# Performance work log

Measured on AMD Instinct MI355X. Metric: run time of the kernel, lower is better.

## Reference

```python
import jax, jax.numpy as jnp
import numpy as np
import math

Z, N = 4, 128
EMB, L0, MLPH, GEO = 16, 32, 64, 64
NB, NH = 32, 128
C = MLPH + GEO
BETA, MAXR = 5.0, 10.0
Y0 = 0.5 / math.sqrt(math.pi)  # spherical harmonic l=0


def setup_inputs() -> dict:
    key = jax.random.key(0)
    ks = jax.random.split(key, 24)
    g = lambda i, s: jax.random.normal(ks[i], s, jnp.float32)
    inp = {}
    inp['features'] = jax.random.randint(ks[0], (Z, N, 1), 0, 6)
    inp['geometry'] = g(1, (Z, N, 3))
    inp['mask'] = jnp.ones((Z, N), jnp.float32)
    emb = g(2, (6, EMB))
    inp['emb'] = emb.at[5].set(0.0)  # padding_idx=5
    # radial MLP weights per conv layer (basis->h->h->mul_out*mul_in)
    inp['r0w0'] = g(3, (NB, NH)); inp['r0w1'] = g(4, (NH, NH)); inp['r0w2'] = g(5, (NH, L0 * EMB))
    inp['r1w0'] = g(6, (NB, NH)); inp['r1w1'] = g(7, (NH, NH)); inp['r1w2'] = g(8, (NH, L0 * L0))
    inp['r2w0'] = g(9, (NB, NH)); inp['r2w1'] = g(10, (NH, NH)); inp['r2w2'] = g(11, (NH, MLPH * L0))
    # ResnetPointnet (3 -> GEO per atom, two residual FC blocks)
    inp['pn_w0'] = g(12, (3, GEO)) * 0.3; inp['pn_b0'] = jnp.zeros((GEO,), jnp.float32)
    inp['pn_w1a'] = g(13, (GEO, GEO)) * 0.1; inp['pn_b1a'] = jnp.zeros((GEO,), jnp.float32)
    inp['pn_w1b'] = g(14, (GEO, GEO)) * 0.1; inp['pn_b1b'] = jnp.zeros((GEO,), jnp.float32)
    inp['pn_w2a'] = g(15, (GEO, GEO)) * 0.1; inp['pn_b2a'] = jnp.zeros((GEO,), jnp.float32)
    inp['pn_w2b'] = g(16, (GEO, GEO)) * 0.1; inp['pn_b2b'] = jnp.zeros((GEO,), jnp.float32)
    # output MLP + per-atom BatchNorm1d(natoms) params
    inp['e1_w'] = g(17, (C, C)) * 0.05; inp['e1_b'] = jnp.zeros((C,), jnp.float32)
    inp['bn1_g'] = jnp.ones((N,), jnp.float32); inp['bn1_b'] = jnp.zeros((N,), jnp.float32)
    inp['e2_w'] = g(18, (C, 2 * C)) * 0.05; inp['e2_b'] = jnp.zeros((2 * C,), jnp.float32)
    inp['bn2_g'] = jnp.ones((N,), jnp.float32); inp['bn2_b'] = jnp.zeros((N,), jnp.float32)
    return inp


def _sp(x):
    return jax.nn.softplus(BETA * x) / BETA


def _ssp(x):
    return _sp(x) - math.log(2.0) / BETA


def _leaky(x):
    return jnp.where(x > 0, x, 0.2 * x)


def _radial(radii, w0, w1, w2):
    # CosineBasisModel: smooth cosine^2 bumps then small MLP (e3nn-style /sqrt(fan_in))
    centers = jnp.linspace(0.0, MAXR, NB)
    step = centers[1] - centers[0]
    x = (radii[..., None] - centers) / step
    basis = jnp.where(jnp.abs(x) < 1.0, jnp.cos(0.5 * jnp.pi * x) ** 2, 0.0)  # [z,a,b,NB]
    h = _ssp(basis @ w0 / math.sqrt(NB))
    h = _ssp(h @ w1 / math.sqrt(NH))
    return h @ w2 / math.sqrt(NH)  # [z,a,b,dout*din]


def _bn(x, gamma, beta):
    # torch BatchNorm1d(natoms) on [Z, natoms, C]: normalize over (Z, C) per atom slot
    mu = jnp.mean(x, axis=(0, 2), keepdims=True)
    var = jnp.var(x, axis=(0, 2), keepdims=True)
    xn = (x - mu) * jax.lax.rsqrt(var + 1e-5)
    return xn * gamma[None, :, None] + beta[None, :, None]


def reference(features, geometry, mask, emb,
              r0w0, r0w1, r0w2, r1w0, r1w1, r1w2, r2w0, r2w1, r2w2,
              pn_w0, pn_b0, pn_w1a, pn_b1a, pn_w1b, pn_b1b,
              pn_w2a, pn_b2a, pn_w2b, pn_b2b,
              e1_w, e1_b, bn1_g, bn1_b, e2_w, e2_b, bn2_g, bn2_b):
    # constants(): pairwise geometry, detached in the original
    diff = jax.lax.stop_gradient(geometry[:, None, :, :] - geometry[:, :, None, :])  # [z,a,b,3]
    radii = jnp.linalg.norm(diff, axis=-1)  # [z,a,b]

    # ResnetPointnet: per-atom geometric features
    net = geometry @ pn_w0 + pn_b0
    for (wa, ba, wb, bb) in ((pn_w1a, pn_b1a, pn_w1b, pn_b1b), (pn_w2a, pn_b2a, pn_w2b, pn_b2b)):
        dx = jax.nn.relu(net) @ wa + ba
        dx = jax.nn.relu(dx) @ wb + bb
        net = net + dx
    geo_pn = net * mask[..., None]  # [z,n,GEO]

    # embedding
    f = emb[features[..., 0]]  # [z,n,EMB]

    # equivariant kernel-conv layers; all reps are l=0 so Y = Y0 constant
    dims = ((EMB, L0, r0w0, r0w1, r0w2), (L0, L0, r1w0, r1w1, r1w2), (L0, MLPH, r2w0, r2w1, r2w2))
    for (din, dout, w0, w1, w2) in dims:
        f = f / math.sqrt(N)
        K = _radial(radii, w0, w1, w2).reshape(Z, N, N, dout, din)
        f = jnp.einsum('zabij,zbj,zb->zai', K, f, mask) * Y0
        f = _sp(f)               # GatedBlock with all-scalar Rs -> scalar act only
        f = f * mask[..., None]

    feat = jnp.concatenate([f, geo_pn], axis=2)  # [z,n,C]
    x = _leaky(_bn(feat @ e1_w + e1_b, bn1_g, bn1_b))
    x = _leaky(_bn(x @ e2_w + e2_b, bn2_g, bn2_b))
    out = jnp.sum(x * mask[..., None], axis=1)  # Aggregate(axis=1, sum)
    return out  # [Z, 2*C]
```

## Files before the change

### kernel.cpp

```cpp
#include <hip/hip_runtime.h>
#include <math.h>

#define Zc   4
#define Nc   128
#define EMBc 16
#define L0c  32
#define MLPHc 64
#define GEOc 64
#define NBc  32
#define NHc  128
#define Cc   128
#define SLc  64

typedef float  f32x4  __attribute__((ext_vector_type(4)));
typedef short  bf16x8 __attribute__((ext_vector_type(8)));

union FragU {
    bf16x8 v;
    unsigned short u[8];
    uint2 q2[2];
};

__device__ __forceinline__ float sp5(float x){
    float y = 5.0f * x;
    float t = fabsf(y);
    return (fmaxf(y, 0.0f) + log1pf(__expf(-t))) * 0.2f;
}
__device__ __forceinline__ float ssp5f(float x){
    float y = 5.0f * x;
    float e = __expf(-fabsf(y));
    return (fmaxf(y, 0.0f) + __logf(1.0f + e)) * 0.2f - 0.13862943611198906f;
}

__device__ __forceinline__ unsigned short f2bf(float f){
    unsigned int u = __float_as_uint(f);
    unsigned int r = (u + 0x7FFFu + ((u >> 16) & 1u)) >> 16;
    return (unsigned short)r;
}

__device__ __forceinline__ int kmap(int l, int e){
    return 4*((l >> 4) & 3) + (e & 3) + 16*(e >> 2);
}

__global__ __launch_bounds__(256) void k_packw(
    const float* __restrict__ w00, const float* __restrict__ w10,
    const float* __restrict__ w01, const float* __restrict__ w11,
    const float* __restrict__ w02, const float* __restrict__ w12,
    unsigned short* __restrict__ packs)
{
    int layer = blockIdx.y;
    const float* w0s = (layer == 0) ? w00 : (layer == 1) ? w01 : w02;
    const float* w1s = (layer == 0) ? w10 : (layer == 1) ? w11 : w12;
    unsigned short* p0 = packs + layer*4096;
    unsigned short* p1 = packs + 12288 + layer*16384;
    int idx = blockIdx.x*256 + threadIdx.x;
    if (idx < 4096){
        int t8 = idx >> 9, l = (idx >> 3) & 63, e = idx & 7;
        int k = kmap(l, e);
        int n = (t8 << 4) + (l & 15);
        p0[idx] = f2bf(w0s[k*NHc + n] * 0.17677669529663687f);
    } else {
        int j = idx - 4096;
        int fid = j >> 9, l = (j >> 3) & 63, e = j & 7;
        int kk = fid >> 3, t8 = fid & 7;
        int k = 32*kk + kmap(l, e);
        int n = 16*t8 + (l & 15);
        p1[j] = f2bf(w1s[k*NHc + n] * 0.08838834764831845f);
    }
}

__global__ __launch_bounds__(64) void k_pointnet(
    const float* __restrict__ geom, const float* __restrict__ mask,
    const float* __restrict__ pw0, const float* __restrict__ pb0,
    const float* __restrict__ w1a, const float* __restrict__ b1a,
    const float* __restrict__ w1b, const float* __restrict__ b1b,
    const float* __restrict__ w2a, const float* __restrict__ b2a,
    const float* __restrict__ w2b, const float* __restrict__ b2b,
    const int*   __restrict__ features, const float* __restrict__ emb,
    float* __restrict__ geo_pn, float* __restrict__ f0)
{
    int zn = blockIdx.x;
    int c  = threadIdx.x;
    __shared__ float cur[GEOc];
    __shared__ float tmp[GEOc];
    float gx = geom[zn*3+0], gy = geom[zn*3+1], gz = geom[zn*3+2];
    float v = fmaf(gx, pw0[0*GEOc+c], fmaf(gy, pw0[1*GEOc+c], fmaf(gz, pw0[2*GEOc+c], pb0[c])));
    const float* WA[2] = {w1a, w2a}; const float* BA[2] = {b1a, b2a};
    const float* WB[2] = {w1b, w2b}; const float* BB[2] = {b1b, b2b};
    #pragma unroll
    for (int blk = 0; blk < 2; blk++){
        cur[c] = v;
        __syncthreads();
        float s = BA[blk][c];
        for (int k = 0; k < GEOc; k++) s = fmaf(fmaxf(cur[k], 0.0f), WA[blk][k*GEOc+c], s);
        tmp[c] = s;
        __syncthreads();
        float s2 = BB[blk][c];
        for (int k = 0; k < GEOc; k++) s2 = fmaf(fmaxf(tmp[k], 0.0f), WB[blk][k*GEOc+c], s2);
        v = v + s2;
        __syncthreads();
    }
    geo_pn[zn*GEOc + c] = v * mask[zn];
    if (c < EMBc){
        int fi = features[zn];
        f0[zn*EMBc + c] = emb[fi*EMBc + c];
    }
}

template<int DIN, int DOUT>
__global__ __launch_bounds__(256) void k_gmat(
    const float* __restrict__ f, const float* __restrict__ mask,
    const float* __restrict__ w2, unsigned short* __restrict__ gt)
{
    __shared__ float fsh[8][DIN];
    int t   = threadIdx.x;
    int zb0 = blockIdx.x * 8;
    if (t < 8*DIN){
        int r = t / DIN, j = t % DIN;
        int zb = zb0 + r;
        fsh[r][j] = f[zb*DIN + j] * mask[zb] * 0.0022038655607334227f;
    }
    __syncthreads();
    int mi = blockIdx.y * 256 + t;
    int m_ = mi & (NHc-1);
    int i_ = mi >> 7;
    const float* wrow = w2 + (size_t)(m_*DOUT + i_) * DIN;
    float s[8];
    #pragma unroll
    for (int r = 0; r < 8; r++) s[r] = 0.0f;
    #pragma unroll
    for (int j4 = 0; j4 < DIN/4; j4++){
        float4 w = *reinterpret_cast<const float4*>(&wrow[j4*4]);
        #pragma unroll
        for (int q = 0; q < 4; q++){
            float wv = reinterpret_cast<const float*>(&w)[q];
            int j = j4*4 + q;
            #pragma unroll
            for (int r = 0; r < 8; r++)
                s[r] = fmaf(fsh[r][j], wv, s[r]);
        }
    }
    int z = zb0 >> 7;
    #pragma unroll
    for (int r = 0; r < 8; r++){
        int b = (zb0 + r) & (Nc-1);
        gt[((size_t)z*DOUT + i_)*(Nc*NHc) + b*NHc + m_] = f2bf(s[r]);
    }
}

template<int DIN, int DOUT>
__global__ __launch_bounds__(256) void k_egmat(
    const float* __restrict__ part, const float* __restrict__ mask,
    const float* __restrict__ w2, unsigned short* __restrict__ gt)
{
    __shared__ float fsh[8][DIN];
    int t   = threadIdx.x;
    int zb0 = blockIdx.x * 8;
    for (int idx = t; idx < 8*DIN; idx += 256){
        int r = idx / DIN, j = idx % DIN;
        int zb = zb0 + r;
        float s = 0.0f;
        #pragma unroll
        for (int sl = 0; sl < SLc; sl++)
            s += part[(size_t)sl*(Zc*Nc*DIN) + zb*DIN + j];
        float m = mask[zb];
        fsh[r][j] = sp5(s) * m * m * 0.0022038655607334227f;
    }
    __syncthreads();
    int mi = blockIdx.y * 256 + t;
    int m_ = mi & (NHc-1);
    int i_ = mi >> 7;
    const float* wrow = w2 + (size_t)(m_*DOUT + i_) * DIN;
    float s[8];
    #pragma unroll
    for (int r = 0; r < 8; r++) s[r] = 0.0f;
    #pragma unroll
    for (int j4 = 0; j4 < DIN/4; j4++){
        float4 w = *reinterpret_cast<const float4*>(&wrow[j4*4]);
        #pragma unroll
        for (int q = 0; q < 4; q++){
            float wv = reinterpret_cast<const float*>(&w)[q];
            int j = j4*4 + q;
            #pragma unroll
            for (int r = 0; r < 8; r++)
                s[r] = fmaf(fsh[r][j], wv, s[r]);
        }
    }
    int z = zb0 >> 7;
    #pragma unroll
    for (int r = 0; r < 8; r++){
        int b = (zb0 + r) & (Nc-1);
        gt[((size_t)z*DOUT + i_)*(Nc*NHc) + b*NHc + m_] = f2bf(s[r]);
    }
}

__global__ __launch_bounds__(256) void k_pairmlp(
    const float* __restrict__ geom,
    const unsigned short* __restrict__ packs,
    unsigned short* __restrict__ h2all)
{
    __shared__ unsigned short h1s[64*128];
    char* lb = (char*)h1s;
    int layer = blockIdx.y;
    const unsigned short* wp0 = packs + layer*4096;
    const unsigned short* wp1 = packs + 12288 + layer*16384;
    unsigned short* h2 = h2all + (size_t)layer * (Zc*Nc*Nc*NHc);

    int t   = threadIdx.x;
    int w   = t >> 6;
    int l   = t & 63;
    int g16 = l >> 4;
    int c   = l & 15;
    int p0  = blockIdx.x * 64;
    int z   = p0 >> 14;
    int a   = (p0 >> 7) & 127;
    int b0  = p0 & 127;

    int bp = b0 + 16*w + c;
    float ax = geom[(z*Nc + a)*3 + 0];
    float ay = geom[(z*Nc + a)*3 + 1];
    float az = geom[(z*Nc + a)*3 + 2];
    float dx = geom[(z*Nc + bp)*3 + 0] - ax;
    float dy = geom[(z*Nc + bp)*3 + 1] - ay;
    float dz = geom[(z*Nc + bp)*3 + 2] - az;
    float rm = sqrtf(dx*dx + dy*dy + dz*dz);

    FragU af;
    #pragma unroll
    for (int e = 0; e < 8; e++){
        int k = kmap(l, e);
        float x = rm*3.1f - (float)k;
        float v = 0.0f;
        if (fabsf(x) < 1.0f){ float cc = __cosf(1.57079632679f*x); v = cc*cc; }
        af.u[e] = f2bf(v);
    }

    f32x4 acc[8];
    #pragma unroll
    for (int t8 = 0; t8 < 8; t8++) acc[t8] = (f32x4){0.f,0.f,0.f,0.f};
    #pragma unroll
    for (int t8 = 0; t8 < 8; t8++){
        bf16x8 bf = *reinterpret_cast<const bf16x8*>(wp0 + ((t8*64 + l) << 3));
        acc[t8] = __builtin_amdgcn_mfma_f32_16x16x32_bf16(af.v, bf, acc[t8], 0, 0, 0);
    }
    #pragma unroll
    for (int t8 = 0; t8 < 8; t8++){
        #pragma unroll
        for (int rg = 0; rg < 4; rg++){
            int m = 16*w + 4*g16 + rg;
            int n = 16*t8 + c;
            int off = ((m << 8) + (n << 1)) ^ ((m & 7) << 4);
            *(unsigned short*)(lb + off) = f2bf(ssp5f(acc[t8][rg]));
        }
    }
    __syncthreads();

    f32x4 acc2[8];
    #pragma unroll
    for (int t8 = 0; t8 < 8; t8++) acc2[t8] = (f32x4){0.f,0.f,0.f,0.f};
    int mrow = 16*w + c;
    int sw   = (mrow & 7) << 4;
    #pragma unroll
    for (int kk = 0; kk < 4; kk++){
        int ob = (mrow << 8) + (kk << 6) + (g16 << 3);
        FragU a2;
        a2.q2[0] = *(const uint2*)(lb + (ob ^ sw));
        a2.q2[1] = *(const uint2*)(lb + ((ob + 32) ^ sw));
        #pragma unroll
        for (int t8 = 0; t8 < 8; t8++){
            bf16x8 bf = *reinterpret_cast<const bf16x8*>(wp1 + (((kk*8 + t8)*64 + l) << 3));
            acc2[t8] = __builtin_amdgcn_mfma_f32_16x16x32_bf16(a2.v, bf, acc2[t8], 0, 0, 0);
        }
    }
    size_t rowbase = ((size_t)((z*Nc + a)*Nc + b0)) * NHc;
    #pragma unroll
    for (int t8 = 0; t8 < 8; t8++){
        #pragma unroll
        for (int rg = 0; rg < 4; rg++){
            int m = 16*w + 4*g16 + rg;
            h2[rowbase + (size_t)m*NHc + 16*t8 + c] = f2bf(ssp5f(acc2[t8][rg]));
        }
    }
}

template<int DOUT>
__global__ __launch_bounds__(256) void k_gemm3m(
    const unsigned short* __restrict__ h2, const unsigned short* __restrict__ gt,
    float* __restrict__ partial)
{
    __shared__ unsigned short Ash[64*256];
    __shared__ unsigned short Bsh[DOUT*256];
    int t = threadIdx.x;
    int w = t >> 6, l = t & 63;
    int g16 = l >> 4, c16 = l & 15;
    int s  = blockIdx.x;
    int at = blockIdx.y;
    int z  = blockIdx.z;
    int a0 = at*64;
    int k0 = s*256;

    {
        const unsigned short* src = h2 + ((size_t)(z*Nc + a0))*(Nc*NHc) + k0;
        #pragma unroll
        for (int it = 0; it < 8; it++){
            int idx = it*256 + t;
            int r = idx >> 5, c8 = idx & 31;
            uint4 v = *reinterpret_cast<const uint4*>(src + (size_t)r*(Nc*NHc) + c8*8);
            int byte = (r*512 + c8*16) ^ ((r & 7) << 4);
            *reinterpret_cast<uint4*>((char*)Ash + byte) = v;
        }
    }
    {
        const unsigned short* src = gt + ((size_t)z*DOUT)*(Nc*NHc) + k0;
        #pragma unroll
        for (int it = 0; it < DOUT/8; it++){
            int idx = it*256 + t;
            int r = idx >> 5, c8 = idx & 31;
            uint4 v = *reinterpret_cast<const uint4*>(src + (size_t)r*(Nc*NHc) + c8*8);
            int byte = (r*512 + c8*16) ^ ((r & 7) << 4);
            *reinterpret_cast<uint4*>((char*)Bsh + byte) = v;
        }
    }
    __syncthreads();

    constexpr int NT = DOUT/16;
    f32x4 acc[NT];
    #pragma unroll
    for (int nt = 0; nt < NT; nt++) acc[nt] = (f32x4){0.f,0.f,0.f,0.f};
    char* Ab = (char*)Ash; char* Bb = (char*)Bsh;
    int ar  = 16*w + c16;
    int asw = (ar & 7) << 4;
    #pragma unroll
    for (int ks = 0; ks < 8; ks++){
        FragU afr;
        int abyte = ar*512 + ks*64 + g16*8;
        afr.q2[0] = *(const uint2*)(Ab + (abyte ^ asw));
        afr.q2[1] = *(const uint2*)(Ab + ((abyte + 32) ^ asw));
        #pragma unroll
        for (int nt = 0; nt < NT; nt++){
            int br  = nt*16 + c16;
            int bsw = (br & 7) << 4;
            int bbyte = br*512 + ks*64 + g16*8;
            FragU bfr;
            bfr.q2[0] = *(const uint2*)(Bb + (bbyte ^ bsw));
            bfr.q2[1] = *(const uint2*)(Bb + ((bbyte + 32) ^ bsw));
            acc[nt] = __builtin_amdgcn_mfma_f32_16x16x32_bf16(afr.v, bfr.v, acc[nt], 0, 0, 0);
        }
    }
    #pragma unroll
    for (int nt = 0; nt < NT; nt++){
        #pragma unroll
        for (int rg = 0; rg < 4; rg++){
            int a = a0 + 16*w + 4*g16 + rg;
            int i = nt*16 + c16;
            partial[(((size_t)s*Zc + z)*Nc + a)*DOUT + i] = acc[nt][rg];
        }
    }
}

__global__ __launch_bounds__(128) void k_x1f(
    const float* __restrict__ part, const float* __restrict__ mask,
    const float* __restrict__ geo_pn,
    const float* __restrict__ w, const float* __restrict__ b,
    float* __restrict__ x1)
{
    int zn = blockIdx.x;
    int c  = threadIdx.x;
    __shared__ float feat[Cc];
    float fv;
    if (c < MLPHc){
        float s = 0.0f;
        #pragma unroll
        for (int sl = 0; sl < SLc; sl++)
            s += part[(size_t)sl*(Zc*Nc*MLPHc) + zn*MLPHc + c];
        fv = sp5(s) * mask[zn];
    } else {
        fv = geo_pn[zn*GEOc + (c - MLPHc)];
    }
    feat[c] = fv;
    __syncthreads();
    float s = b[c];
    for (int k = 0; k < Cc; k++) s = fmaf(feat[k], w[k*Cc + c], s);
    x1[zn*Cc + c] = s;
}

__global__ __launch_bounds__(256) void k_bnx2(
    const float* __restrict__ x1, const float* __restrict__ g1,
    const float* __restrict__ b1, const float* __restrict__ e2w,
    const float* __restrict__ e2b, float* __restrict__ x2)
{
    int n = blockIdx.x;
    int t = threadIdx.x;
    __shared__ float xsh[Zc][Cc];
    __shared__ float ssum[4], ssq[4];
    float sum = 0.0f, sq = 0.0f;
    for (int idx = t; idx < Zc*Cc; idx += 256){
        int z = idx >> 7, c = idx & 127;
        float v = x1[((size_t)z*Nc + n)*Cc + c];
        xsh[z][c] = v;
        sum += v; sq += v*v;
    }
    #pragma unroll
    for (int off = 32; off > 0; off >>= 1){
        sum += __shfl_down(sum, off);
        sq  += __shfl_down(sq,  off);
    }
    if ((t & 63) == 0){ ssum[t >> 6] = sum; ssq[t >> 6] = sq; }
    __syncthreads();
    float tot  = ssum[0] + ssum[1] + ssum[2] + ssum[3];
    float totq = ssq[0]  + ssq[1]  + ssq[2]  + ssq[3];
    const float inv = 1.0f / (float)(Zc*Cc);
    float mu   = tot * inv;
    float var  = totq * inv - mu*mu;
    float rstd = rsqrtf(var + 1e-5f);
    float ga = g1[n], be = b1[n];
    for (int idx = t; idx < Zc*Cc; idx += 256){
        int z = idx >> 7, c = idx & 127;
        float v = (xsh[z][c] - mu) * rstd * ga + be;
        xsh[z][c] = v > 0.0f ? v : 0.2f*v;
    }
    __syncthreads();
    #pragma unroll
    for (int z = 0; z < Zc; z++){
        float s = e2b[t];
        for (int k = 0; k < Cc; k++) s = fmaf(xsh[z][k], e2w[k*2*Cc + t], s);
        x2[((size_t)z*Nc + n)*2*Cc + t] = s;
    }
}

template<int CC>
__global__ __launch_bounds__(256) void k_bn(
    float* __restrict__ x, const float* __restrict__ gamma,
    const float* __restrict__ beta)
{
    int n = blockIdx.x;
    int t = threadIdx.x;
    __shared__ float ssum[4], ssq[4];
    float sum = 0.0f, sq = 0.0f;
    for (int idx = t; idx < Zc*CC; idx += 256){
        int z = idx / CC, c = idx % CC;
        float v = x[((size_t)z*Nc + n)*CC + c];
        sum += v; sq += v*v;
    }
    #pragma unroll
    for (int off = 32; off > 0; off >>= 1){
        sum += __shfl_down(sum, off);
        sq  += __shfl_down(sq,  off);
    }
    if ((t & 63) == 0){ ssum[t >> 6] = sum; ssq[t >> 6] = sq; }
    __syncthreads();
    float tot  = ssum[0] + ssum[1] + ssum[2] + ssum[3];
    float totq = ssq[0]  + ssq[1]  + ssq[2]  + ssq[3];
    const float inv = 1.0f / (float)(Zc*CC);
    float mu   = tot * inv;
    float var  = totq * inv - mu*mu;
    float rstd = rsqrtf(var + 1e-5f);
    float ga = gamma[n], be = beta[n];
    for (int idx = t; idx < Zc*CC; idx += 256){
        int z = idx / CC, c = idx % CC;
        size_t o = ((size_t)z*Nc + n)*CC + c;
        float v = (x[o] - mu) * rstd * ga + be;
        x[o] = v > 0.0f ? v : 0.2f*v;
    }
}

__global__ __launch_bounds__(256) void k_out(
    const float* __restrict__ x2n, const float* __restrict__ mask,
    float* __restrict__ out)
{
    int z = blockIdx.x;
    int c = threadIdx.x;
    float s = 0.0f;
    for (int n = 0; n < Nc; n++)
        s += x2n[((size_t)z*Nc + n)*2*Cc + c] * mask[z*Nc + n];
    out[z*2*Cc + c] = s;
}

extern "C" void kernel_launch(void* const* d_in, const int* in_sizes, int n_in,
                              void* d_out, int out_size, void* d_ws, size_t ws_size,
                              hipStream_t stream)
{
    const int*   features = (const int*)  d_in[0];
    const float* geom     = (const float*)d_in[1];
    const float* mask     = (const float*)d_in[2];
    const float* emb      = (const float*)d_in[3];
    const float* rw[3][3] = {
        {(const float*)d_in[4],  (const float*)d_in[5],  (const float*)d_in[6]},
        {(const float*)d_in[7],  (const float*)d_in[8],  (const float*)d_in[9]},
        {(const float*)d_in[10], (const float*)d_in[11], (const float*)d_in[12]}};
    const float* pw0 = (const float*)d_in[13]; const float* pb0 = (const float*)d_in[14];
    const float* w1a = (const float*)d_in[15]; const float* b1a = (const float*)d_in[16];
    const float* w1b = (const float*)d_in[17]; const float* b1b = (const float*)d_in[18];
    const float* w2a = (const float*)d_in[19]; const float* b2a = (const float*)d_in[20];
    const float* w2b = (const float*)d_in[21]; const float* b2b = (const float*)d_in[22];
    const float* e1w = (const float*)d_in[23]; const float* e1b = (const float*)d_in[24];
    const float* bn1g= (const float*)d_in[25]; const float* bn1b= (const float*)d_in[26];
    const float* e2w = (const float*)d_in[27]; const float* e2b = (const float*)d_in[28];
    const float* bn2g= (const float*)d_in[29]; const float* bn2b= (const float*)d_in[30];

    float* ws = (float*)d_ws;
    unsigned short* h2buf = (unsigned short*)ws;
    unsigned short* gt    = (unsigned short*)(ws + 12582912);
    float* part   = ws + 12582912 + 2097152;
    float* f0     = part + 2097152;
    float* geo_pn = f0 + 8192;
    float* x1     = geo_pn + 32768;
    float* x2     = x1 + 65536;
    unsigned short* packs = (unsigned short*)(x2 + 131072);
    (void)ws_size; (void)in_sizes; (void)n_in; (void)out_size;

    const size_t H2L = (size_t)Zc*Nc*Nc*NHc;

    k_packw<<<dim3(80, 3), 256, 0, stream>>>(rw[0][0], rw[0][1], rw[1][0], rw[1][1],
                                             rw[2][0], rw[2][1], packs);
    k_pointnet<<<Zc*Nc, 64, 0, stream>>>(geom, mask, pw0, pb0, w1a, b1a, w1b, b1b,
                                         w2a, b2a, w2b, b2b, features, emb, geo_pn, f0);
    k_pairmlp<<<dim3(Zc*Nc*Nc/64, 3), 256, 0, stream>>>(geom, packs, h2buf);

    k_gmat<16,32><<<dim3(Zc*Nc/8, (NHc*32)/256), 256, 0, stream>>>(f0, mask, rw[0][2], gt);
    k_gemm3m<32><<<dim3(SLc,2,Zc), 256, 0, stream>>>(h2buf, gt, part);
    k_egmat<32,32><<<dim3(Zc*Nc/8, (NHc*32)/256), 256, 0, stream>>>(part, mask, rw[1][2], gt);
    k_gemm3m<32><<<dim3(SLc,2,Zc), 256, 0, stream>>>(h2buf + H2L, gt, part);
    k_egmat<32,64><<<dim3(Zc*Nc/8, (NHc*64)/256), 256, 0, stream>>>(part, mask, rw[2][2], gt);
    k_gemm3m<64><<<dim3(SLc,2,Zc), 256, 0, stream>>>(h2buf + 2*H2L, gt, part);

    k_x1f<<<Zc*Nc, 128, 0, stream>>>(part, mask, geo_pn, e1w, e1b, x1);
    k_bnx2<<<Nc, 256, 0, stream>>>(x1, bn1g, bn1b, e2w, e2b, x2);
    k_bn<2*Cc><<<Nc, 256, 0, stream>>>(x2, bn2g, bn2b);
    k_out<<<Zc, 256, 0, stream>>>(x2, mask, (float*)d_out);
}
```

Baseline: 168.7 us.

## Hoist partial-sum epilogue out of gmat, fold softplus scale into weights

The fused k_egmat re-reduced the 64 partial slices for every blockIdx.y tile, so the same reduction was repeated many times over. This moves that reduction plus softplus and mask scaling into a separate k_epi kernel that runs once per element, and turns k_gmat into a plain consumer. The embedding mask and scale move into k_pointnet. The beta=5 factor is folded into the packed pair-MLP weights. bf16 rounding now uses v_cvt_pk_bf16_f32 instead of integer bit arithmetic. The cost is one extra kernel launch per layer and an extra small f1/f2 buffer round-trip.

```diff
diff --git a/kernel.cpp b/kernel.cpp
--- a/kernel.cpp
+++ b/kernel.cpp
@@ -26,12 +26,17 @@
     float t = fabsf(y);
     return (fmaxf(y, 0.0f) + log1pf(__expf(-t))) * 0.2f;
 }
-__device__ __forceinline__ float ssp5f(float x){
-    float y = 5.0f * x;
+__device__ __forceinline__ float ssp5_post(float y){
     float e = __expf(-fabsf(y));
-    return (fmaxf(y, 0.0f) + __logf(1.0f + e)) * 0.2f - 0.13862943611198906f;
-}
-
+    float u = fmaxf(y, 0.0f) + __logf(1.0f + e);
+    return fmaf(0.2f, u, -0.13862943611198906f);
+}
+
+__device__ __forceinline__ unsigned int cvtpk_bf16(float a, float b){
+    unsigned int r;
+    asm("v_cvt_pk_bf16_f32 %0, %1, %2" : "=v"(r) : "v"(a), "v"(b));
+    return r;
+}
 __device__ __forceinline__ unsigned short f2bf(float f){
     unsigned int u = __float_as_uint(f);
     unsigned int r = (u + 0x7FFFu + ((u >> 16) & 1u)) >> 16;
@@ -58,14 +63,14 @@
         int t8 = idx >> 9, l = (idx >> 3) & 63, e = idx & 7;
         int k = kmap(l, e);
         int n = (t8 << 4) + (l & 15);
-        p0[idx] = f2bf(w0s[k*NHc + n] * 0.17677669529663687f);
+        p0[idx] = f2bf(w0s[k*NHc + n] * 0.8838834764831844f);
     } else {
         int j = idx - 4096;
         int fid = j >> 9, l = (j >> 3) & 63, e = j & 7;
         int kk = fid >> 3, t8 = fid & 7;
         int k = 32*kk + kmap(l, e);
         int n = 16*t8 + (l & 15);
-        p1[j] = f2bf(w1s[k*NHc + n] * 0.08838834764831845f);
+        p1[j] = f2bf(w1s[k*NHc + n] * 0.4419417382415922f);
     }
 }
 
@@ -103,22 +108,36 @@
     geo_pn[zn*GEOc + c] = v * mask[zn];
     if (c < EMBc){
         int fi = features[zn];
-        f0[zn*EMBc + c] = emb[fi*EMBc + c];
-    }
+        f0[zn*EMBc + c] = emb[fi*EMBc + c] * mask[zn] * 0.0022038655607334227f;
+    }
+}
+
+template<int DIN>
+__global__ __launch_bounds__(256) void k_epi(
+    const float* __restrict__ part, const float* __restrict__ mask,
+    float* __restrict__ fprep)
+{
+    int idx = blockIdx.x*256 + threadIdx.x;
+    if (idx >= Zc*Nc*DIN) return;
+    int zn = idx / DIN;
+    float s = 0.0f;
+    #pragma unroll
+    for (int sl = 0; sl < SLc; sl++) s += part[(size_t)sl*(Zc*Nc*DIN) + idx];
+    float m = mask[zn];
+    fprep[idx] = sp5(s) * m * m * 0.0022038655607334227f;
 }
 
 template<int DIN, int DOUT>
 __global__ __launch_bounds__(256) void k_gmat(
-    const float* __restrict__ f, const float* __restrict__ mask,
-    const float* __restrict__ w2, unsigned short* __restrict__ gt)
+    const float* __restrict__ f, const float* __restrict__ w2,
+    unsigned short* __restrict__ gt)
 {
     __shared__ float fsh[8][DIN];
     int t   = threadIdx.x;
     int zb0 = blockIdx.x * 8;
     if (t < 8*DIN){
         int r = t / DIN, j = t % DIN;
-        int zb = zb0 + r;
-        fsh[r][j] = f[zb*DIN + j] * mask[zb] * 0.0022038655607334227f;
+        fsh[r][j] = f[(zb0 + r)*DIN + j];
     }
     __syncthreads();
     int mi = blockIdx.y * 256 + t;
@@ -144,53 +163,7 @@
     #pragma unroll
     for (int r = 0; r < 8; r++){
         int b = (zb0 + r) & (Nc-1);
-        gt[((size_t)z*DOUT + i_)*(Nc*NHc) + b*NHc + m_] = f2bf(s[r]);
-    }
-}
-
-template<int DIN, int DOUT>
-__global__ __launch_bounds__(256) void k_egmat(
-    const float* __restrict__ part, const float* __restrict__ mask,
-    const float* __restrict__ w2, unsigned short* __restrict__ gt)
-{
-    __shared__ float fsh[8][DIN];
-    int t   = threadIdx.x;
-    int zb0 = blockIdx.x * 8;
-    for (int idx = t; idx < 8*DIN; idx += 256){
-        int r = idx / DIN, j = idx % DIN;
-        int zb = zb0 + r;
-        float s = 0.0f;
-        #pragma unroll
-        for (int sl = 0; sl < SLc; sl++)
-            s += part[(size_t)sl*(Zc*Nc*DIN) + zb*DIN + j];
-        float m = mask[zb];
-        fsh[r][j] = sp5(s) * m * m * 0.0022038655607334227f;
-    }
-    __syncthreads();
-    int mi = blockIdx.y * 256 + t;
-    int m_ = mi & (NHc-1);
-    int i_ = mi >> 7;
-    const float* wrow = w2 + (size_t)(m_*DOUT + i_) * DIN;
-    float s[8];
-    #pragma unroll
-    for (int r = 0; r < 8; r++) s[r] = 0.0f;
-    #pragma unroll
-    for (int j4 = 0; j4 < DIN/4; j4++){
-        float4 w = *reinterpret_cast<const float4*>(&wrow[j4*4]);
-        #pragma unroll
-        for (int q = 0; q < 4; q++){
-            float wv = reinterpret_cast<const float*>(&w)[q];
-            int j = j4*4 + q;
-            #pragma unroll
-            for (int r = 0; r < 8; r++)
-                s[r] = fmaf(fsh[r][j], wv, s[r]);
-        }
-    }
-    int z = zb0 >> 7;
-    #pragma unroll
-    for (int r = 0; r < 8; r++){
-        int b = (zb0 + r) & (Nc-1);
-        gt[((size_t)z*DOUT + i_)*(Nc*NHc) + b*NHc + m_] = f2bf(s[r]);
+        gt[((size_t)z*DOUT + i_)*(Nc*NHc) + b*NHc + m_] = (unsigned short)cvtpk_bf16(s[r], s[r]);
     }
 }
 
@@ -229,10 +202,10 @@
     #pragma unroll
     for (int e = 0; e < 8; e++){
         int k = kmap(l, e);
-        float x = rm*3.1f - (float)k;
+        float x = fmaf(rm, 3.1f, -(float)k);
         float v = 0.0f;
         if (fabsf(x) < 1.0f){ float cc = __cosf(1.57079632679f*x); v = cc*cc; }
-        af.u[e] = f2bf(v);
+        af.u[e] = (unsigned short)cvtpk_bf16(v, v);
     }
 
     f32x4 acc[8];
@@ -250,7 +223,7 @@
             int m = 16*w + 4*g16 + rg;
             int n = 16*t8 + c;
             int off = ((m << 8) + (n << 1)) ^ ((m & 7) << 4);
-            *(unsigned short*)(lb + off) = f2bf(ssp5f(acc[t8][rg]));
+            *(unsigned short*)(lb + off) = (unsigned short)cvtpk_bf16(ssp5_post(acc[t8][rg]), 0.0f);
         }
     }
     __syncthreads();
@@ -278,7 +251,8 @@
         #pragma unroll
         for (int rg = 0; rg < 4; rg++){
             int m = 16*w + 4*g16 + rg;
-            h2[rowbase + (size_t)m*NHc + 16*t8 + c] = f2bf(ssp5f(acc2[t8][rg]));
+            h2[rowbase + (size_t)m*NHc + 16*t8 + c] =
+                (unsigned short)cvtpk_bf16(ssp5_post(acc2[t8][rg]), 0.0f);
         }
     }
 }
@@ -503,7 +477,9 @@
     unsigned short* gt    = (unsigned short*)(ws + 12582912);
     float* part   = ws + 12582912 + 2097152;
     float* f0     = part + 2097152;
-    float* geo_pn = f0 + 8192;
+    float* f1     = f0 + 8192;
+    float* f2     = f1 + 16384;
+    float* geo_pn = f2 + 16384;
     float* x1     = geo_pn + 32768;
     float* x2     = x1 + 65536;
     unsigned short* packs = (unsigned short*)(x2 + 131072);
@@ -517,11 +493,13 @@
                                          w2a, b2a, w2b, b2b, features, emb, geo_pn, f0);
     k_pairmlp<<<dim3(Zc*Nc*Nc/64, 3), 256, 0, stream>>>(geom, packs, h2buf);
 
-    k_gmat<16,32><<<dim3(Zc*Nc/8, (NHc*32)/256), 256, 0, stream>>>(f0, mask, rw[0][2], gt);
+    k_gmat<16,32><<<dim3(Zc*Nc/8, (NHc*32)/256), 256, 0, stream>>>(f0, rw[0][2], gt);
     k_gemm3m<32><<<dim3(SLc,2,Zc), 256, 0, stream>>>(h2buf, gt, part);
-    k_egmat<32,32><<<dim3(Zc*Nc/8, (NHc*32)/256), 256, 0, stream>>>(part, mask, rw[1][2], gt);
+    k_epi<32><<<(Zc*Nc*32 + 255)/256, 256, 0, stream>>>(part, mask, f1);
+    k_gmat<32,32><<<dim3(Zc*Nc/8, (NHc*32)/256), 256, 0, stream>>>(f1, rw[1][2], gt);
     k_gemm3m<32><<<dim3(SLc,2,Zc), 256, 0, stream>>>(h2buf + H2L, gt, part);
-    k_egmat<32,64><<<dim3(Zc*Nc/8, (NHc*64)/256), 256, 0, stream>>>(part, mask, rw[2][2], gt);
+    k_epi<32><<<(Zc*Nc*32 + 255)/256, 256, 0, stream>>>(part, mask, f2);
+    k_gmat<32,64><<<dim3(Zc*Nc/8, (NHc*64)/256), 256, 0, stream>>>(f2, rw[2][2], gt);
     k_gemm3m<64><<<dim3(SLc,2,Zc), 256, 0, stream>>>(h2buf + 2*H2L, gt, part);
 
     k_x1f<<<Zc*Nc, 128, 0, stream>>>(part, mask, geo_pn, e1w, e1b, x1);
```

New measurement: 172.9 us. 1.02x slower.
